# Performance work log

Hardware: AMD Instinct MI355X
Metric: run time of the kernel (lower is better)

The kernel has to match this reference:

```python
import jax, jax.numpy as jnp
import numpy as np

K_CODES = 64
EPS_LN = 1e-5


def hamilton_product(p, q):
    # p, q: [..., D] with D = 4*Q, components ordered (r, i, j, k)
    Q = p.shape[-1] // 4
    pr, pi, pj, pk = (p[..., :Q], p[..., Q:2*Q], p[..., 2*Q:3*Q], p[..., 3*Q:])
    qr, qi, qj, qk = (q[..., :Q], q[..., Q:2*Q], q[..., 2*Q:3*Q], q[..., 3*Q:])
    out_r = pr * qr - pi * qi - pj * qj - pk * qk
    out_i = pr * qi + pi * qr + pj * qk - pk * qj
    out_j = pr * qj - pi * qk + pj * qr + pk * qi
    out_k = pr * qk + pi * qj - pj * qi + pk * qr
    return jnp.concatenate([out_r, out_i, out_j, out_k], axis=-1)


def quaternion_linear(x, w4, b):
    # w4: [4, Qo, Qi] stacked (r, i, j, k); builds Hamilton block matrix [D, D]
    r, i, j, k = w4[0], w4[1], w4[2], w4[3]
    W = jnp.block([[r, -i, -j, -k],
                   [i,  r, -k,  j],
                   [j,  k,  r, -i],
                   [k, -j,  i,  r]])
    return x @ W.T + b


def quaternion_layernorm(x, gamma, beta):
    # independent LayerNorm over each quaternion component (4 chunks of size Q)
    Qd = x.shape[-1] // 4
    xs = x.reshape(*x.shape[:-1], 4, Qd)
    mu = xs.mean(axis=-1, keepdims=True)
    var = ((xs - mu) ** 2).mean(axis=-1, keepdims=True)
    xn = (xs - mu) / jnp.sqrt(var + EPS_LN)
    out = xn * gamma + beta  # gamma/beta: [4, Qd]
    return out.reshape(*x.shape[:-1], 4 * Qd)


def setup_inputs() -> dict:
    key = jax.random.key(0)
    ks = jax.random.split(key, 8)
    B, N, D, m = 8, 4096, 512, 3
    Qd = D // 4
    q = jax.random.normal(ks[0], (B, N, D), dtype=jnp.float32)
    assign_idx = jax.random.randint(ks[1], (B, N, m), 0, K_CODES)
    assign_w = jax.random.uniform(ks[2], (B, N, m), dtype=jnp.float32)
    contribute_mask = jnp.ones((B, N), dtype=jnp.float32)
    scale = 0.5 / np.sqrt(Qd)
    proto_w = jax.random.normal(ks[3], (4, Qd, Qd), dtype=jnp.float32) * scale
    proto_b = jax.random.normal(ks[4], (D,), dtype=jnp.float32) * 0.01
    upd_w = jax.random.normal(ks[5], (4, Qd, Qd), dtype=jnp.float32) * scale
    upd_b = jax.random.normal(ks[6], (D,), dtype=jnp.float32) * 0.01
    ln_gamma = jnp.ones((4, Qd), dtype=jnp.float32)
    ln_beta = jnp.zeros((4, Qd), dtype=jnp.float32)
    return {"q": q, "assign_idx": assign_idx, "assign_w": assign_w,
            "contribute_mask": contribute_mask, "proto_w": proto_w,
            "proto_b": proto_b, "upd_w": upd_w, "upd_b": upd_b,
            "ln_gamma": ln_gamma, "ln_beta": ln_beta}


def reference(q, assign_idx, assign_w, contribute_mask, proto_w, proto_b,
              upd_w, upd_b, ln_gamma, ln_beta):
    B, N, D = q.shape
    m = assign_idx.shape[-1]
    K = K_CODES

    # --- scatter-add prototype aggregation ---
    agg_w = assign_w * contribute_mask[..., None]            # [B, N, m]
    flat_idx = assign_idx.reshape(B, N * m)                  # [B, N*m]
    flat_w = agg_w.reshape(B, N * m, 1)                      # [B, N*m, 1]
    weighted_q = (q[:, :, None, :] * agg_w[..., None]).reshape(B, N * m, D)

    seg = lambda v, idx: jax.ops.segment_sum(v, idx, num_segments=K)
    proto = jax.vmap(seg)(weighted_q, flat_idx)              # [B, K, D]
    weight_sum = jax.vmap(seg)(flat_w, flat_idx)             # [B, K, 1]
    proto = proto / (weight_sum + 1e-6)
    proto = quaternion_linear(proto, proto_w, proto_b)       # [B, K, D]

    # --- gather prototypes per observation + Hamilton routing ---
    proto_per_obs = jax.vmap(lambda p, idx: p[idx])(proto, assign_idx)  # [B, N, m, D]
    routed = hamilton_product(q[:, :, None, :], proto_per_obs)          # [B, N, m, D]
    msg = (routed * assign_w[..., None]).sum(axis=2)                    # [B, N, D]
    msg = quaternion_linear(msg, upd_w, upd_b)

    q_new = quaternion_layernorm(q + msg, ln_gamma, ln_beta)
    return q_new, proto
```

## Files before the change

### kernel.cpp

```cpp
#include <hip/hip_runtime.h>
#include <hip/hip_bf16.h>

#define B_ 8
#define N_ 4096
#define D_ 512
#define K_ 64
#define QD_ 128

typedef float f32x4 __attribute__((ext_vector_type(4)));
typedef short short8 __attribute__((ext_vector_type(8)));
typedef unsigned short u16;
typedef unsigned int u32;

__device__ __forceinline__ u16 f2bf(float f) {
  u32 u = __float_as_uint(f);
  return (u16)((u + 0x7fffu + ((u >> 16) & 1u)) >> 16);
}
__device__ __forceinline__ float bf2f(u16 h) {
  return __uint_as_float((u32)h << 16);
}

__device__ __forceinline__ void load8f(const float* p, float* r) {
  float4 a = *(const float4*)(p);
  float4 b = *(const float4*)(p + 4);
  r[0] = a.x; r[1] = a.y; r[2] = a.z; r[3] = a.w;
  r[4] = b.x; r[5] = b.y; r[6] = b.z; r[7] = b.w;
}

__device__ __forceinline__ void store_comp(char* msgL, int row, int u, int s,
                                           int swz, const float* m) {
  uint4 val;
  val.x = (u32)f2bf(m[0]) | ((u32)f2bf(m[1]) << 16);
  val.y = (u32)f2bf(m[2]) | ((u32)f2bf(m[3]) << 16);
  val.z = (u32)f2bf(m[4]) | ((u32)f2bf(m[5]) << 16);
  val.w = (u32)f2bf(m[6]) | ((u32)f2bf(m[7]) << 16);
  const int byte = (row * 1024 + u * 256 + s * 16) ^ swz;
  *(uint4*)(msgL + byte) = val;
}

__global__ __launch_bounds__(256) void k_wexp_frag(
    const float* __restrict__ uw, const float* __restrict__ pw,
    u16* __restrict__ uwf, u16* __restrict__ pwf) {
  const int gid = blockIdx.x * 256 + threadIdx.x;
  const int sel = gid >> 18;
  const int idx = gid & ((1 << 18) - 1);
  const int e = idx & 7;
  const int lane = (idx >> 3) & 63;
  const int ks = (idx >> 9) & 15;
  const int cf = idx >> 13;
  const int col = (cf >> 3) * 128 + (cf & 7) * 16 + (lane & 15);
  const int v = ks * 32 + (lane >> 4) * 8 + e;
  const int u = col >> 7, a = col & 127, c = v >> 7, bb = v & 127;
  const int   matT[4][4] = {{0,1,2,3},{1,0,3,2},{2,3,0,1},{3,2,1,0}};
  const float sgnT[4][4] = {{1.f,-1.f,-1.f,-1.f},{1.f,1.f,-1.f,1.f},
                            {1.f,1.f,1.f,-1.f},{1.f,-1.f,1.f,1.f}};
  const float* w4 = sel ? pw : uw;
  u16* dst = sel ? pwf : uwf;
  dst[idx] = f2bf(sgnT[u][c] * w4[matT[u][c] * QD_ * QD_ + a * QD_ + bb]);
}

__global__ __launch_bounds__(256) void k_bldA(
    const int* __restrict__ aidx, const float* __restrict__ aw,
    const float* __restrict__ mask, u16* __restrict__ A) {
  const int gid = blockIdx.x * 256 + threadIdx.x;
  const int b = gid >> 12, n = gid & 4095;
  const size_t ib = (size_t)gid * 3;
  const int k0 = aidx[ib], k1 = aidx[ib + 1], k2 = aidx[ib + 2];
  const float mk = mask[gid];
  float w0 = aw[ib] * mk, w1 = aw[ib + 1] * mk, w2 = aw[ib + 2] * mk;
  bool skip1 = false, skip2 = false;
  if (k1 == k0) { w0 += w1; skip1 = true; }
  if (k2 == k0) { w0 += w2; skip2 = true; }
  else if (k2 == k1 && !skip1) { w1 += w2; skip2 = true; }
  u16* Ab = A + (size_t)b * K_ * N_;
#pragma unroll
  for (int k = 0; k < K_; ++k) Ab[(size_t)k * N_ + n] = 0;
  Ab[(size_t)k0 * N_ + n] = f2bf(w0);
  if (!skip1) Ab[(size_t)k1 * N_ + n] = f2bf(w1);
  if (!skip2) Ab[(size_t)k2 * N_ + n] = f2bf(w2);
}

__global__ __launch_bounds__(256) void k_gemmA(
    const u16* __restrict__ A, const float* __restrict__ q,
    float* __restrict__ proto_raw, float* __restrict__ wsum) {
  __shared__ __align__(16) u16 Bt[128 * 64];
  const int t = threadIdx.x;
  const int kc = blockIdx.x;
  const int dq = blockIdx.y;
  const int b = blockIdx.z;
  const int n_base = kc * 256;
  const u16* Ab = A + (size_t)b * K_ * N_;
  const float* qb = q + ((size_t)b * N_ + n_base) * D_ + dq * 128;

  const int lane = t & 63, wv = t >> 6;
  const int g = lane >> 4, l16 = lane & 15;
  const int sn = t >> 2, sdq = (t & 3) * 32;

  f32x4 acc[4][2];
#pragma unroll
  for (int mt = 0; mt < 4; ++mt)
#pragma unroll
    for (int nt = 0; nt < 2; ++nt) { f32x4 z = {0.f,0.f,0.f,0.f}; acc[mt][nt] = z; }

  float4 pre[8];
#pragma unroll
  for (int e = 0; e < 8; ++e)
    pre[e] = *(const float4*)(qb + (size_t)sn * D_ + sdq + e * 4);

  for (int sub = 0; sub < 4; ++sub) {
    __syncthreads();
#pragma unroll
    for (int e = 0; e < 8; ++e) {
      const float4 v = pre[e];
#pragma unroll
      for (int x = 0; x < 4; ++x) {
        const int d = sdq + e * 4 + x;
        const float fv = (x == 0) ? v.x : (x == 1) ? v.y : (x == 2) ? v.z : v.w;
        const int byte = (d * 128 + sn * 2) ^ ((d & 7) << 4);
        *(u16*)((char*)Bt + byte) = f2bf(fv);
      }
    }
    float4 nxt[8];
    if (sub < 3) {
#pragma unroll
      for (int e = 0; e < 8; ++e)
        nxt[e] = *(const float4*)(qb + (size_t)((sub + 1) * 64 + sn) * D_ + sdq + e * 4);
    }
    __syncthreads();
    const int n0 = n_base + sub * 64;
#pragma unroll
    for (int ks = 0; ks < 2; ++ks) {
      short8 bfrag[2];
#pragma unroll
      for (int nt = 0; nt < 2; ++nt) {
        const int d = wv * 32 + nt * 16 + l16;
        const int byte = (d * 128 + (ks * 32 + g * 8) * 2) ^ ((d & 7) << 4);
        bfrag[nt] = *(const short8*)((const char*)Bt + byte);
      }
#pragma unroll
      for (int mt = 0; mt < 4; ++mt) {
        const short8 afr = *(const short8*)(Ab + (size_t)(mt * 16 + l16) * N_ +
                                            n0 + ks * 32 + g * 8);
#pragma unroll
        for (int nt = 0; nt < 2; ++nt)
          acc[mt][nt] = __builtin_amdgcn_mfma_f32_16x16x32_bf16(afr, bfrag[nt], acc[mt][nt], 0, 0, 0);
      }
    }
#pragma unroll
    for (int e = 0; e < 8; ++e) pre[e] = nxt[e];
  }

#pragma unroll
  for (int mt = 0; mt < 4; ++mt)
#pragma unroll
    for (int nt = 0; nt < 2; ++nt)
#pragma unroll
      for (int rg = 0; rg < 4; ++rg) {
        const int code = mt * 16 + g * 4 + rg;
        const int d = dq * 128 + wv * 32 + nt * 16 + l16;
        atomicAdd(&proto_raw[((size_t)b * K_ + code) * D_ + d], acc[mt][nt][rg]);
      }

  if (dq == 0) {
    const int k = t >> 2, part = t & 3;
    const u16* ap = Ab + (size_t)k * N_ + n_base + part * 64;
    float s = 0.f;
#pragma unroll
    for (int i = 0; i < 8; ++i) {
      const short8 v = *(const short8*)(ap + i * 8);
#pragma unroll
      for (int e = 0; e < 8; ++e) s += bf2f((u16)v[e]);
    }
    s += __shfl_xor(s, 1);
    s += __shfl_xor(s, 2);
    if (part == 0) atomicAdd(&wsum[b * K_ + k], s);
  }
}

__global__ __launch_bounds__(256) void k_proto_mfma(
    const float* __restrict__ proto_raw, const float* __restrict__ wsum,
    const u16* __restrict__ pwf, const float* __restrict__ pb,
    float* __restrict__ proto_t, float* __restrict__ out_proto) {
  __shared__ __align__(16) u16 msgL[16 * 512];
  __shared__ float invs[16];
  const int t = threadIdx.x;
  const size_t R0 = (size_t)blockIdx.x * 16;
  if (t < 16) invs[t] = 1.f / (wsum[R0 + t] + 1e-6f);
  __syncthreads();

  {
    const int s = t & 15, row = t >> 4;
    const float iv = invs[row];
    const float* base = proto_raw + (R0 + row) * D_;
    const int swz = (row & 7) << 4;
#pragma unroll
    for (int u = 0; u < 4; ++u) {
      float m[8];
      load8f(base + u * 128 + s * 8, m);
#pragma unroll
      for (int e = 0; e < 8; ++e) m[e] *= iv;
      store_comp((char*)msgL, row, u, s, swz, m);
    }
  }
  __syncthreads();

  const int lane = t & 63, wv = t >> 6;
  const int g = lane >> 4, l16 = lane & 15;
  f32x4 acc[8];
#pragma unroll
  for (int f = 0; f < 8; ++f) { f32x4 z = {0.f,0.f,0.f,0.f}; acc[f] = z; }
#pragma unroll 4
  for (int ks = 0; ks < 16; ++ks) {
    const int arow = l16;
    const short8 a = *(const short8*)((const char*)msgL +
        ((arow * 1024 + ks * 64 + g * 16) ^ ((arow & 7) << 4)));
#pragma unroll
    for (int f = 0; f < 8; ++f) {
      const short8 bv = *(const short8*)(pwf +
          ((size_t)((wv * 8 + f) * 16 + ks) * 64 + lane) * 8);
      acc[f] = __builtin_amdgcn_mfma_f32_16x16x32_bf16(a, bv, acc[f], 0, 0, 0);
    }
  }

#pragma unroll
  for (int f = 0; f < 8; ++f) {
    const int col = wv * 128 + f * 16 + l16;
    const float pbv = pb[col];
#pragma unroll
    for (int rg = 0; rg < 4; ++rg) {
      const size_t row = R0 + g * 4 + rg;
      const float v = acc[f][rg] + pbv;
      proto_t[row * D_ + col] = v;
      out_proto[row * D_ + col] = v;
    }
  }
}

__global__ __launch_bounds__(256) void k_main8(
    const float* __restrict__ q, const int* __restrict__ aidx,
    const float* __restrict__ aw, const float* __restrict__ proto_t,
    const u16* __restrict__ uwf, const float* __restrict__ ub,
    const float* __restrict__ gamma, const float* __restrict__ beta,
    float* __restrict__ out_q) {
  __shared__ __align__(16) u16 msgL[32 * 512];
  const int t = threadIdx.x;
  const size_t R0 = (size_t)blockIdx.x * 32;

  {
    const int s = t & 15, rowHalf = t >> 4;
    int kks[2][3]; float wws[2][3];
#pragma unroll
    for (int p = 0; p < 2; ++p) {
      const size_t gr = R0 + p * 16 + rowHalf;
      const int* ip = aidx + gr * 3;
      const float* wp = aw + gr * 3;
#pragma unroll
      for (int j = 0; j < 3; ++j) { kks[p][j] = ip[j]; wws[p][j] = wp[j]; }
    }
#pragma unroll
    for (int p = 0; p < 2; ++p) {
      const int row = p * 16 + rowHalf;
      const size_t gr = R0 + row;
      const int b = (int)(gr >> 12);
      const float* qp = q + gr * D_ + s * 8;
      float qr_[8], qi_[8], qj_[8], qk_[8];
      load8f(qp, qr_); load8f(qp + 128, qi_);
      load8f(qp + 256, qj_); load8f(qp + 384, qk_);
      float Pr[8], Pi[8], Pj[8], Pk[8];
#pragma unroll
      for (int e = 0; e < 8; ++e) { Pr[e] = Pi[e] = Pj[e] = Pk[e] = 0.f; }
#pragma unroll
      for (int j = 0; j < 3; ++j) {
        const float w = wws[p][j];
        const float* pp = proto_t + (size_t)(b * K_ + kks[p][j]) * D_ + s * 8;
        float pr[8], pi[8], pj[8], pk[8];
        load8f(pp, pr); load8f(pp + 128, pi);
        load8f(pp + 256, pj); load8f(pp + 384, pk);
#pragma unroll
        for (int e = 0; e < 8; ++e) {
          Pr[e] += w * pr[e]; Pi[e] += w * pi[e];
          Pj[e] += w * pj[e]; Pk[e] += w * pk[e];
        }
      }
      const int swz = (row & 7) << 4;
      float m[8];
#pragma unroll
      for (int e = 0; e < 8; ++e)
        m[e] = qr_[e]*Pr[e] - qi_[e]*Pi[e] - qj_[e]*Pj[e] - qk_[e]*Pk[e];
      store_comp((char*)msgL, row, 0, s, swz, m);
#pragma unroll
      for (int e = 0; e < 8; ++e)
        m[e] = qr_[e]*Pi[e] + qi_[e]*Pr[e] + qj_[e]*Pk[e] - qk_[e]*Pj[e];
      store_comp((char*)msgL, row, 1, s, swz, m);
#pragma unroll
      for (int e = 0; e < 8; ++e)
        m[e] = qr_[e]*Pj[e] - qi_[e]*Pk[e] + qj_[e]*Pr[e] + qk_[e]*Pi[e];
      store_comp((char*)msgL, row, 2, s, swz, m);
#pragma unroll
      for (int e = 0; e < 8; ++e)
        m[e] = qr_[e]*Pk[e] + qi_[e]*Pj[e] - qj_[e]*Pi[e] + qk_[e]*Pr[e];
      store_comp((char*)msgL, row, 3, s, swz, m);
    }
  }
  __syncthreads();

  const int lane = t & 63, c4 = t >> 6;
  const int g = lane >> 4, l16 = lane & 15;
  f32x4 acc[2][8];
#pragma unroll
  for (int st = 0; st < 2; ++st)
#pragma unroll
    for (int f = 0; f < 8; ++f) { f32x4 z = {0.f,0.f,0.f,0.f}; acc[st][f] = z; }
#pragma unroll 2
  for (int ks = 0; ks < 16; ++ks) {
    short8 bfr[8];
#pragma unroll
    for (int f = 0; f < 8; ++f)
      bfr[f] = *(const short8*)(uwf +
          ((size_t)((c4 * 8 + f) * 16 + ks) * 64 + lane) * 8);
#pragma unroll
    for (int st = 0; st < 2; ++st) {
      const int arow = st * 16 + l16;
      const short8 a = *(const short8*)((const char*)msgL +
          ((arow * 1024 + ks * 64 + g * 16) ^ ((arow & 7) << 4)));
#pragma unroll
      for (int f = 0; f < 8; ++f)
        acc[st][f] = __builtin_amdgcn_mfma_f32_16x16x32_bf16(a, bfr[f], acc[st][f], 0, 0, 0);
    }
  }

  const int colQ = c4 * 128;
#pragma unroll
  for (int st = 0; st < 2; ++st)
#pragma unroll
    for (int f = 0; f < 8; ++f) {
      const int col = colQ + f * 16 + l16;
      const float ubv = ub[col];
#pragma unroll
      for (int rg = 0; rg < 4; ++rg) {
        const size_t row = R0 + st * 16 + g * 4 + rg;
        acc[st][f][rg] += ubv + q[row * D_ + col];
      }
    }
#pragma unroll
  for (int st = 0; st < 2; ++st)
#pragma unroll
    for (int rg = 0; rg < 4; ++rg) {
      float s = 0.f;
#pragma unroll
      for (int f = 0; f < 8; ++f) s += acc[st][f][rg];
      s += __shfl_xor(s, 1); s += __shfl_xor(s, 2);
      s += __shfl_xor(s, 4); s += __shfl_xor(s, 8);
      const float mean = s * 0.0078125f;
      float sq = 0.f;
#pragma unroll
      for (int f = 0; f < 8; ++f) {
        const float d = acc[st][f][rg] - mean; sq += d * d;
      }
      sq += __shfl_xor(sq, 1); sq += __shfl_xor(sq, 2);
      sq += __shfl_xor(sq, 4); sq += __shfl_xor(sq, 8);
      const float rstd = rsqrtf(sq * 0.0078125f + 1e-5f);
      const size_t row = R0 + st * 16 + g * 4 + rg;
#pragma unroll
      for (int f = 0; f < 8; ++f) {
        const int col = colQ + f * 16 + l16;
        const float xn = (acc[st][f][rg] - mean) * rstd;
        out_q[row * D_ + col] = xn * gamma[col] + beta[col];
      }
    }
}

extern "C" void kernel_launch(void* const* d_in, const int* in_sizes, int n_in,
                              void* d_out, int out_size, void* d_ws, size_t ws_size,
                              hipStream_t stream) {
  const float* q     = (const float*)d_in[0];
  const int*   aidx  = (const int*)d_in[1];
  const float* aw    = (const float*)d_in[2];
  const float* mask  = (const float*)d_in[3];
  const float* pw    = (const float*)d_in[4];
  const float* pb    = (const float*)d_in[5];
  const float* uw    = (const float*)d_in[6];
  const float* ub    = (const float*)d_in[7];
  const float* gamma = (const float*)d_in[8];
  const float* beta  = (const float*)d_in[9];

  char* ws = (char*)d_ws;
  const size_t MB = 1 << 20;
  float* proto_raw = (float*)ws;
  float* wsum      = (float*)(ws + MB);
  u16*   A         = (u16*)(ws + MB + 4096);
  float* proto_t   = (float*)(ws + 5 * MB + 4096);
  u16*   uwf       = (u16*)(ws + 6 * MB + 4096);
  u16*   pwf       = (u16*)(ws + 6 * MB + 4096 + (512 << 10));

  float* out_q = (float*)d_out;
  float* out_proto = out_q + (size_t)B_ * N_ * D_;

  hipMemsetAsync(ws, 0, MB + 4096, stream);
  k_wexp_frag<<<2048, 256, 0, stream>>>(uw, pw, uwf, pwf);
  k_bldA<<<128, 256, 0, stream>>>(aidx, aw, mask, A);
  k_gemmA<<<dim3(16, 4, 8), 256, 0, stream>>>(A, q, proto_raw, wsum);
  k_proto_mfma<<<32, 256, 0, stream>>>(proto_raw, wsum, pwf, pb, proto_t, out_proto);
  k_main8<<<1024, 256, 0, stream>>>(q, aidx, aw, proto_t, uwf, ub, gamma, beta, out_q);
}
```

Before: 131.6 us.

## Merge prep kernels, double gemmA grid, split B-fragment loads in main GEMM

Measured after the change: 152.2 us. +15.6%, slower.

```diff
diff --git a/kernel.cpp b/kernel.cpp
--- a/kernel.cpp
+++ b/kernel.cpp
@@ -38,46 +38,46 @@
   *(uint4*)(msgL + byte) = val;
 }
 
-__global__ __launch_bounds__(256) void k_wexp_frag(
+__global__ __launch_bounds__(256) void k_prep(
     const float* __restrict__ uw, const float* __restrict__ pw,
-    u16* __restrict__ uwf, u16* __restrict__ pwf) {
-  const int gid = blockIdx.x * 256 + threadIdx.x;
-  const int sel = gid >> 18;
-  const int idx = gid & ((1 << 18) - 1);
-  const int e = idx & 7;
-  const int lane = (idx >> 3) & 63;
-  const int ks = (idx >> 9) & 15;
-  const int cf = idx >> 13;
-  const int col = (cf >> 3) * 128 + (cf & 7) * 16 + (lane & 15);
-  const int v = ks * 32 + (lane >> 4) * 8 + e;
-  const int u = col >> 7, a = col & 127, c = v >> 7, bb = v & 127;
-  const int   matT[4][4] = {{0,1,2,3},{1,0,3,2},{2,3,0,1},{3,2,1,0}};
-  const float sgnT[4][4] = {{1.f,-1.f,-1.f,-1.f},{1.f,1.f,-1.f,1.f},
-                            {1.f,1.f,1.f,-1.f},{1.f,-1.f,1.f,1.f}};
-  const float* w4 = sel ? pw : uw;
-  u16* dst = sel ? pwf : uwf;
-  dst[idx] = f2bf(sgnT[u][c] * w4[matT[u][c] * QD_ * QD_ + a * QD_ + bb]);
-}
-
-__global__ __launch_bounds__(256) void k_bldA(
+    u16* __restrict__ uwf, u16* __restrict__ pwf,
     const int* __restrict__ aidx, const float* __restrict__ aw,
     const float* __restrict__ mask, u16* __restrict__ A) {
-  const int gid = blockIdx.x * 256 + threadIdx.x;
-  const int b = gid >> 12, n = gid & 4095;
-  const size_t ib = (size_t)gid * 3;
-  const int k0 = aidx[ib], k1 = aidx[ib + 1], k2 = aidx[ib + 2];
-  const float mk = mask[gid];
-  float w0 = aw[ib] * mk, w1 = aw[ib + 1] * mk, w2 = aw[ib + 2] * mk;
-  bool skip1 = false, skip2 = false;
-  if (k1 == k0) { w0 += w1; skip1 = true; }
-  if (k2 == k0) { w0 += w2; skip2 = true; }
-  else if (k2 == k1 && !skip1) { w1 += w2; skip2 = true; }
-  u16* Ab = A + (size_t)b * K_ * N_;
-#pragma unroll
-  for (int k = 0; k < K_; ++k) Ab[(size_t)k * N_ + n] = 0;
-  Ab[(size_t)k0 * N_ + n] = f2bf(w0);
-  if (!skip1) Ab[(size_t)k1 * N_ + n] = f2bf(w1);
-  if (!skip2) Ab[(size_t)k2 * N_ + n] = f2bf(w2);
+  if (blockIdx.x < 2048) {
+    const int gid = blockIdx.x * 256 + threadIdx.x;
+    const int sel = gid >> 18;
+    const int idx = gid & ((1 << 18) - 1);
+    const int e = idx & 7;
+    const int lane = (idx >> 3) & 63;
+    const int ks = (idx >> 9) & 15;
+    const int cf = idx >> 13;
+    const int col = (cf >> 3) * 128 + (cf & 7) * 16 + (lane & 15);
+    const int v = ks * 32 + (lane >> 4) * 8 + e;
+    const int u = col >> 7, a = col & 127, c = v >> 7, bb = v & 127;
+    const int   matT[4][4] = {{0,1,2,3},{1,0,3,2},{2,3,0,1},{3,2,1,0}};
+    const float sgnT[4][4] = {{1.f,-1.f,-1.f,-1.f},{1.f,1.f,-1.f,1.f},
+                              {1.f,1.f,1.f,-1.f},{1.f,-1.f,1.f,1.f}};
+    const float* w4 = sel ? pw : uw;
+    u16* dst = sel ? pwf : uwf;
+    dst[idx] = f2bf(sgnT[u][c] * w4[matT[u][c] * QD_ * QD_ + a * QD_ + bb]);
+  } else {
+    const int gid = (blockIdx.x - 2048) * 256 + threadIdx.x;
+    const int b = gid >> 12, n = gid & 4095;
+    const size_t ib = (size_t)gid * 3;
+    const int k0 = aidx[ib], k1 = aidx[ib + 1], k2 = aidx[ib + 2];
+    const float mk = mask[gid];
+    float w0 = aw[ib] * mk, w1 = aw[ib + 1] * mk, w2 = aw[ib + 2] * mk;
+    bool skip1 = false, skip2 = false;
+    if (k1 == k0) { w0 += w1; skip1 = true; }
+    if (k2 == k0) { w0 += w2; skip2 = true; }
+    else if (k2 == k1 && !skip1) { w1 += w2; skip2 = true; }
+    u16* Ab = A + (size_t)b * K_ * N_;
+#pragma unroll
+    for (int k = 0; k < K_; ++k) Ab[(size_t)k * N_ + n] = 0;
+    Ab[(size_t)k0 * N_ + n] = f2bf(w0);
+    if (!skip1) Ab[(size_t)k1 * N_ + n] = f2bf(w1);
+    if (!skip2) Ab[(size_t)k2 * N_ + n] = f2bf(w2);
+  }
 }
 
 __global__ __launch_bounds__(256) void k_gemmA(
@@ -88,7 +88,7 @@
   const int kc = blockIdx.x;
   const int dq = blockIdx.y;
   const int b = blockIdx.z;
-  const int n_base = kc * 256;
+  const int n_base = kc * 128;
   const u16* Ab = A + (size_t)b * K_ * N_;
   const float* qb = q + ((size_t)b * N_ + n_base) * D_ + dq * 128;
 
@@ -107,7 +107,7 @@
   for (int e = 0; e < 8; ++e)
     pre[e] = *(const float4*)(qb + (size_t)sn * D_ + sdq + e * 4);
 
-  for (int sub = 0; sub < 4; ++sub) {
+  for (int sub = 0; sub < 2; ++sub) {
     __syncthreads();
 #pragma unroll
     for (int e = 0; e < 8; ++e) {
@@ -121,10 +121,10 @@
       }
     }
     float4 nxt[8];
-    if (sub < 3) {
+    if (sub < 1) {
 #pragma unroll
       for (int e = 0; e < 8; ++e)
-        nxt[e] = *(const float4*)(qb + (size_t)((sub + 1) * 64 + sn) * D_ + sdq + e * 4);
+        nxt[e] = *(const float4*)(qb + (size_t)(64 + sn) * D_ + sdq + e * 4);
     }
     __syncthreads();
     const int n0 = n_base + sub * 64;
@@ -163,10 +163,10 @@
 
   if (dq == 0) {
     const int k = t >> 2, part = t & 3;
-    const u16* ap = Ab + (size_t)k * N_ + n_base + part * 64;
+    const u16* ap = Ab + (size_t)k * N_ + n_base + part * 32;
     float s = 0.f;
 #pragma unroll
-    for (int i = 0; i < 8; ++i) {
+    for (int i = 0; i < 4; ++i) {
       const short8 v = *(const short8*)(ap + i * 8);
 #pragma unroll
       for (int e = 0; e < 8; ++e) s += bf2f((u16)v[e]);
@@ -236,7 +236,7 @@
   }
 }
 
-__global__ __launch_bounds__(256) void k_main8(
+__global__ __launch_bounds__(256) void k_main9(
     const float* __restrict__ q, const int* __restrict__ aidx,
     const float* __restrict__ aw, const float* __restrict__ proto_t,
     const u16* __restrict__ uwf, const float* __restrict__ ub,
@@ -313,19 +313,34 @@
     for (int f = 0; f < 8; ++f) { f32x4 z = {0.f,0.f,0.f,0.f}; acc[st][f] = z; }
 #pragma unroll 2
   for (int ks = 0; ks < 16; ++ks) {
-    short8 bfr[8];
-#pragma unroll
-    for (int f = 0; f < 8; ++f)
-      bfr[f] = *(const short8*)(uwf +
-          ((size_t)((c4 * 8 + f) * 16 + ks) * 64 + lane) * 8);
-#pragma unroll
-    for (int st = 0; st < 2; ++st) {
-      const int arow = st * 16 + l16;
-      const short8 a = *(const short8*)((const char*)msgL +
-          ((arow * 1024 + ks * 64 + g * 16) ^ ((arow & 7) << 4)));
-#pragma unroll
-      for (int f = 0; f < 8; ++f)
-        acc[st][f] = __builtin_amdgcn_mfma_f32_16x16x32_bf16(a, bfr[f], acc[st][f], 0, 0, 0);
+    const int arow0 = l16, arow1 = 16 + l16;
+    const short8 a0 = *(const short8*)((const char*)msgL +
+        ((arow0 * 1024 + ks * 64 + g * 16) ^ ((arow0 & 7) << 4)));
+    const short8 a1 = *(const short8*)((const char*)msgL +
+        ((arow1 * 1024 + ks * 64 + g * 16) ^ ((arow1 & 7) << 4)));
+    {
+      short8 bf[4];
+#pragma unroll
+      for (int f = 0; f < 4; ++f)
+        bf[f] = *(const short8*)(uwf +
+            ((size_t)((c4 * 8 + f) * 16 + ks) * 64 + lane) * 8);
+#pragma unroll
+      for (int f = 0; f < 4; ++f) {
+        acc[0][f] = __builtin_amdgcn_mfma_f32_16x16x32_bf16(a0, bf[f], acc[0][f], 0, 0, 0);
+        acc[1][f] = __builtin_amdgcn_mfma_f32_16x16x32_bf16(a1, bf[f], acc[1][f], 0, 0, 0);
+      }
+    }
+    {
+      short8 bf[4];
+#pragma unroll
+      for (int f = 0; f < 4; ++f)
+        bf[f] = *(const short8*)(uwf +
+            ((size_t)((c4 * 8 + 4 + f) * 16 + ks) * 64 + lane) * 8);
+#pragma unroll
+      for (int f = 0; f < 4; ++f) {
+        acc[0][4 + f] = __builtin_amdgcn_mfma_f32_16x16x32_bf16(a0, bf[f], acc[0][4 + f], 0, 0, 0);
+        acc[1][4 + f] = __builtin_amdgcn_mfma_f32_16x16x32_bf16(a1, bf[f], acc[1][4 + f], 0, 0, 0);
+      }
     }
   }
 
@@ -397,9 +412,8 @@
   float* out_proto = out_q + (size_t)B_ * N_ * D_;
 
   hipMemsetAsync(ws, 0, MB + 4096, stream);
-  k_wexp_frag<<<2048, 256, 0, stream>>>(uw, pw, uwf, pwf);
-  k_bldA<<<128, 256, 0, stream>>>(aidx, aw, mask, A);
-  k_gemmA<<<dim3(16, 4, 8), 256, 0, stream>>>(A, q, proto_raw, wsum);
+  k_prep<<<2048 + 128, 256, 0, stream>>>(uw, pw, uwf, pwf, aidx, aw, mask, A);
+  k_gemmA<<<dim3(32, 4, 8), 256, 0, stream>>>(A, q, proto_raw, wsum);
   k_proto_mfma<<<32, 256, 0, stream>>>(proto_raw, wsum, pwf, pb, proto_t, out_proto);
-  k_main8<<<1024, 256, 0, stream>>>(q, aidx, aw, proto_t, uwf, ub, gamma, beta, out_q);
-}
+  k_main9<<<1024, 256, 0, stream>>>(q, aidx, aw, proto_t, uwf, ub, gamma, beta, out_q);
+}
```
